# Performance work log

Hardware: AMD Instinct MI355X
Metric: run time of the kernel (lower is better)

The kernel has to match this reference:

```python
import jax, jax.numpy as jnp
import numpy as np

C, S, H = 64, 2048, 512
ITERATIONS = 3

def squash(x, eps=1e-07):
    # per-vector squash along last dim: (|x|^2/(1+|x|^2)) * x/|x|
    sq = jnp.sum(x * x, axis=-1, keepdims=True)
    safe_norm = jnp.sqrt(sq + eps)
    scale = sq / (1.0 + sq)
    return scale * (x / safe_norm)

def setup_inputs() -> dict:
    key = jax.random.key(0)
    k1, k2 = jax.random.split(key)
    x = jax.random.normal(k1, (C * S, H), dtype=jnp.float32)
    # xavier-normal init for Linear(H, H)
    std = np.sqrt(2.0 / (H + H)).astype(np.float32)
    W_weight = jax.random.normal(k2, (H, H), dtype=jnp.float32) * std
    W_bias = jnp.zeros((H,), dtype=jnp.float32)
    return {"x": x, "W_weight": W_weight, "W_bias": W_bias}

def reference(x, W_weight, W_bias):
    xr = x.reshape(C, S, H)
    # e_ij = squash(Linear(x))  -> [C, S, H]
    e_ij = squash(jnp.einsum('csh,oh->cso', xr, W_weight) + W_bias)
    b_ij = jnp.zeros((C, S), dtype=x.dtype)
    c_i = jnp.zeros((C, H), dtype=x.dtype)
    for _ in range(ITERATIONS):
        d_i = jax.nn.softmax(b_ij, axis=1)[..., None]          # [C, S, 1]
        c_i = squash(jnp.sum(d_i * e_ij, axis=1))              # [C, H]
        b_ij = b_ij + jnp.einsum('csh,ch->cs', e_ij, c_i)      # [C, S]
    return c_i
```

## Files before the change

kernel.cpp:

```cpp
#include <hip/hip_runtime.h>
#include <hip/hip_fp16.h>

#define HDIM 512

typedef __fp16 fp16x2 __attribute__((ext_vector_type(2)));
typedef _Float16 h8 __attribute__((ext_vector_type(8)));
typedef __attribute__((ext_vector_type(4))) float floatx4;

__global__ __launch_bounds__(256) void prep_w_kernel(
    const float* __restrict__ W, _Float16* __restrict__ wf) {
  int i = (blockIdx.x * 256 + threadIdx.x) * 4;
  float4 f = *(const float4*)(W + i);
  wf[i + 0] = (_Float16)f.x;
  wf[i + 1] = (_Float16)f.y;
  wf[i + 2] = (_Float16)f.z;
  wf[i + 3] = (_Float16)f.w;
}

__global__ __launch_bounds__(256) void gemm_kernel(
    const float* __restrict__ x, const _Float16* __restrict__ wf,
    const float* __restrict__ bias, __half* __restrict__ y,
    float* __restrict__ sq) {
  __shared__ _Float16 xs[128 * 64];
  __shared__ _Float16 wsm[2][128 * 64];

  const int tid = threadIdx.x;
  const int lane = tid & 63;
  const int widx = tid >> 6;
  const int wave_m = widx >> 1, wave_n = widx & 1;
  const int lrow = lane & 15, quad = lane >> 4, l7 = lane & 7;

  const int bid = blockIdx.x;
  const int m_blk = ((bid >> 5) << 3) + (bid & 7);
  const int n_blk = (bid >> 3) & 3;
  const int row0 = m_blk * 128;
  const int col0 = n_blk * 128;

  floatx4 acc[4][4];
#pragma unroll
  for (int i = 0; i < 4; ++i)
#pragma unroll
    for (int j = 0; j < 4; ++j) acc[i][j] = (floatx4){0.f, 0.f, 0.f, 0.f};

  const int xm = tid >> 3;
  const int xkg = tid & 7;
  const int wn_sub = lane >> 3;
  const int wphys = lane & 7;

  float4 xr[4][2];
  const float* xbase = x + (size_t)row0 * HDIM + xkg * 8;
#pragma unroll
  for (int p = 0; p < 4; ++p) {
    const float* gp = xbase + (size_t)(p * 32 + xm) * HDIM;
    xr[p][0] = *(const float4*)gp;
    xr[p][1] = *(const float4*)(gp + 4);
  }
#pragma unroll
  for (int q = 0; q < 4; ++q) {
    int i = widx * 4 + q;
    int n_loc = 8 * i + wn_sub;
    int kg_l = wphys ^ (n_loc & 7);
    size_t goff = (size_t)(col0 + n_loc) * HDIM + kg_l * 8;
    __builtin_amdgcn_global_load_lds(
        (const __attribute__((address_space(1))) void*)(wf + goff),
        (__attribute__((address_space(3))) void*)&wsm[0][i * 512], 16, 0, 0);
  }

  for (int kt = 0; kt < 8; ++kt) {
    __syncthreads();
#pragma unroll
    for (int p = 0; p < 4; ++p) {
      int m = p * 32 + xm;
      union { h8 v8; fp16x2 v2[4]; } u;
      u.v2[0] = __builtin_amdgcn_cvt_pkrtz(xr[p][0].x, xr[p][0].y);
      u.v2[1] = __builtin_amdgcn_cvt_pkrtz(xr[p][0].z, xr[p][0].w);
      u.v2[2] = __builtin_amdgcn_cvt_pkrtz(xr[p][1].x, xr[p][1].y);
      u.v2[3] = __builtin_amdgcn_cvt_pkrtz(xr[p][1].z, xr[p][1].w);
      int phys = xkg ^ (m & 7);
      *(h8*)&xs[m * 64 + phys * 8] = u.v8;
    }
    __syncthreads();
    if (kt < 7) {
      const int k1 = (kt + 1) * 64;
      _Float16* wdst = &wsm[(kt + 1) & 1][0];
#pragma unroll
      for (int q = 0; q < 4; ++q) {
        int i = widx * 4 + q;
        int n_loc = 8 * i + wn_sub;
        int kg_l = wphys ^ (n_loc & 7);
        size_t goff = (size_t)(col0 + n_loc) * HDIM + k1 + kg_l * 8;
        __builtin_amdgcn_global_load_lds(
            (const __attribute__((address_space(1))) void*)(wf + goff),
            (__attribute__((address_space(3))) void*)&wdst[i * 512], 16, 0, 0);
      }
#pragma unroll
      for (int p = 0; p < 4; ++p) {
        const float* gp = xbase + (size_t)(p * 32 + xm) * HDIM + k1;
        xr[p][0] = *(const float4*)gp;
        xr[p][1] = *(const float4*)(gp + 4);
      }
    }
    const _Float16* wcur = &wsm[kt & 1][0];
#pragma unroll
    for (int ks = 0; ks < 2; ++ks) {
      int physA = (ks * 4 + quad) ^ l7;
      h8 a[4], bh[4];
#pragma unroll
      for (int mt = 0; mt < 4; ++mt) {
        int r = wave_m * 64 + mt * 16 + lrow;
        a[mt] = *(const h8*)&xs[r * 64 + physA * 8];
      }
#pragma unroll
      for (int nt = 0; nt < 4; ++nt) {
        int c = wave_n * 64 + nt * 16 + lrow;
        bh[nt] = *(const h8*)&wcur[c * 64 + physA * 8];
      }
#pragma unroll
      for (int mt = 0; mt < 4; ++mt)
#pragma unroll
        for (int nt = 0; nt < 4; ++nt)
          acc[mt][nt] = __builtin_amdgcn_mfma_f32_16x16x32_f16(
              a[mt], bh[nt], acc[mt][nt], 0, 0, 0);
    }
  }

  int colg[4];
  float bias_v[4];
#pragma unroll
  for (int nt = 0; nt < 4; ++nt) {
    colg[nt] = col0 + wave_n * 64 + nt * 16 + lrow;
    bias_v[nt] = bias[colg[nt]];
  }
#pragma unroll
  for (int mt = 0; mt < 4; ++mt) {
#pragma unroll
    for (int r = 0; r < 4; ++r) {
      int rowg = row0 + wave_m * 64 + mt * 16 + quad * 4 + r;
      float s = 0.f;
#pragma unroll
      for (int nt = 0; nt < 4; ++nt) {
        float yv = acc[mt][nt][r] + bias_v[nt];
        s += yv * yv;
        y[(size_t)rowg * HDIM + colg[nt]] = __float2half(yv);
      }
      s += __shfl_xor(s, 1, 64);
      s += __shfl_xor(s, 2, 64);
      s += __shfl_xor(s, 4, 64);
      s += __shfl_xor(s, 8, 64);
      if (lrow == 0) atomicAdd(&sq[rowg], s);
    }
  }
}

__global__ __launch_bounds__(256) void kbv_kernel(
    const __half* __restrict__ y, const float* __restrict__ sqbuf,
    float* __restrict__ b, const float* __restrict__ c_buf,
    float* __restrict__ u_part, float* __restrict__ den_part) {
  const int w = threadIdx.x >> 6;
  const int lane = threadIdx.x & 63;
  const int wave_g = blockIdx.x * 4 + w;
  const int cap = wave_g >> 6;
  const int chunk = wave_g & 63;
  const int r0 = cap * 2048 + chunk * 32;

  float c8[8];
  {
    const float4* cp = (const float4*)(c_buf + cap * HDIM + lane * 8);
    float4 ca = cp[0], cb = cp[1];
    c8[0] = ca.x; c8[1] = ca.y; c8[2] = ca.z; c8[3] = ca.w;
    c8[4] = cb.x; c8[5] = cb.y; c8[6] = cb.z; c8[7] = cb.w;
  }
  float u8[8] = {0, 0, 0, 0, 0, 0, 0, 0};
  float den = 0.f;

  union U { int4 v; __half hh[8]; };
  U cur[8], nxt[8];
  const __half* yb = y + (size_t)r0 * HDIM + lane * 8;
#pragma unroll
  for (int j = 0; j < 8; ++j) cur[j].v = *(const int4*)(yb + (size_t)j * HDIM);

#pragma unroll
  for (int g = 0; g < 4; ++g) {
    const int rg = r0 + g * 8;
    if (g < 3) {
#pragma unroll
      for (int j = 0; j < 8; ++j)
        nxt[j].v = *(const int4*)(yb + (size_t)(g * 8 + 8 + j) * HDIM);
    }
    float sc[8], bv[8];
#pragma unroll
    for (int j = 0; j < 8; ++j) {
      float s = sqbuf[rg + j];
      sc[j] = s / ((1.f + s) * sqrtf(s + 1e-7f));
      bv[j] = b[rg + j];
    }
    float dot[8];
#pragma unroll
    for (int j = 0; j < 8; ++j) {
      float d = 0.f;
#pragma unroll
      for (int k = 0; k < 8; ++k) d += __half2float(cur[j].hh[k]) * c8[k];
      dot[j] = d;
    }
#pragma unroll
    for (int s = 1; s < 64; s <<= 1) {
#pragma unroll
      for (int j = 0; j < 8; ++j) dot[j] += __shfl_xor(dot[j], s, 64);
    }
#pragma unroll
    for (int j = 0; j < 8; ++j) {
      float bn = bv[j] + sc[j] * dot[j];
      if (lane == 0) b[rg + j] = bn;
      float wj = __expf(bn);
      den += wj;
      float wsc = wj * sc[j];
#pragma unroll
      for (int k = 0; k < 8; ++k) u8[k] += wsc * __half2float(cur[j].hh[k]);
    }
#pragma unroll
    for (int j = 0; j < 8; ++j) cur[j] = nxt[j];
  }

  __shared__ float lred[4][512];
  __shared__ float ldn[4];
#pragma unroll
  for (int k = 0; k < 8; ++k) lred[w][lane * 8 + k] = u8[k];
  if (lane == 0) ldn[w] = den;
  __syncthreads();
  const int t = threadIdx.x;
  const int blkc = blockIdx.x & 15;
#pragma unroll
  for (int hh = 0; hh < 2; ++hh) {
    int h = hh * 256 + t;
    float v = lred[0][h] + lred[1][h] + lred[2][h] + lred[3][h];
    u_part[((size_t)cap * 16 + blkc) * HDIM + h] = v;
  }
  if (t == 0)
    den_part[cap * 16 + blkc] = ldn[0] + ldn[1] + ldn[2] + ldn[3];
}

__global__ __launch_bounds__(512) void kcsq_kernel(
    const float* __restrict__ u_part, const float* __restrict__ den_part,
    float* __restrict__ out) {
  const int cap = blockIdx.x;
  const int t = threadIdx.x;
  __shared__ float red[512];
  __shared__ float sden;

  if (t < 16) red[t] = den_part[cap * 16 + t];
  __syncthreads();
  if (t == 0) {
    float s = 0.f;
#pragma unroll
    for (int i = 0; i < 16; ++i) s += red[i];
    sden = s;
  }
  __syncthreads();
  const float den = sden;

  float v = 0.f;
  const float* up = u_part + (size_t)cap * 16 * HDIM + t;
#pragma unroll
  for (int ch = 0; ch < 16; ++ch) v += up[ch * HDIM];
  v /= den;

  red[t] = v * v;
  __syncthreads();
  for (int s = 256; s > 0; s >>= 1) {
    if (t < s) red[t] += red[t + s];
    __syncthreads();
  }
  const float sqv = red[0];
  const float scv = sqv / ((1.f + sqv) * sqrtf(sqv + 1e-7f));
  out[cap * HDIM + t] = v * scv;
}

extern "C" void kernel_launch(void* const* d_in, const int* in_sizes, int n_in,
                              void* d_out, int out_size, void* d_ws,
                              size_t ws_size, hipStream_t stream) {
  const float* x = (const float*)d_in[0];
  const float* W = (const float*)d_in[1];
  const float* bias = (const float*)d_in[2];
  float* out = (float*)d_out;
  char* ws = (char*)d_ws;

  __half* y = (__half*)ws;
  float* sq = (float*)(ws + (size_t)134217728);
  float* b = sq + 131072;
  float* c_buf = b + 131072;
  _Float16* wf = (_Float16*)(c_buf + 32768);
  float* u_part = (float*)(wf + 262144);
  float* den_part = u_part + (size_t)64 * 16 * 512;

  (void)hipMemsetAsync(sq, 0,
                       (size_t)(131072 + 131072 + 32768) * sizeof(float),
                       stream);

  prep_w_kernel<<<256, 256, 0, stream>>>(W, wf);
  gemm_kernel<<<4096, 256, 0, stream>>>(x, wf, bias, y, sq);

  for (int it = 0; it < 3; ++it) {
    kbv_kernel<<<1024, 256, 0, stream>>>(y, sq, b, c_buf, u_part, den_part);
    kcsq_kernel<<<64, 512, 0, stream>>>(u_part, den_part,
                                        (it == 2) ? out : c_buf);
  }
}
```

Baseline: 565.8 us.

## Deepen GEMM prefetch pipeline with staggered K start and explicit waitcnt control

The GEMM now double-buffers the x register tiles two k-steps ahead, rotates each block's K starting offset by block index to spread memory traffic, and replaces __syncthreads with a raw lgkmcnt barrier plus hand-placed vmcnt waits so outstanding global loads can overlap MFMA work. The routing kernel's row batch shrinks from 8 to 4 rows per step, which lowers register pressure at the cost of more loop iterations. The hand-written vmcnt counts depend on the exact instruction count the compiler emits and could be wrong if that changes.

```diff
diff --git a/kernel.cpp b/kernel.cpp
--- a/kernel.cpp
+++ b/kernel.cpp
@@ -6,6 +6,13 @@
 typedef __fp16 fp16x2 __attribute__((ext_vector_type(2)));
 typedef _Float16 h8 __attribute__((ext_vector_type(8)));
 typedef __attribute__((ext_vector_type(4))) float floatx4;
+
+__device__ __forceinline__ void lds_barrier() {
+  asm volatile("s_waitcnt lgkmcnt(0)\n\ts_barrier" ::: "memory");
+}
+__device__ __forceinline__ void issue_fence() {
+  asm volatile("" ::: "memory");
+}
 
 __global__ __launch_bounds__(256) void prep_w_kernel(
     const float* __restrict__ W, _Float16* __restrict__ wf) {
@@ -17,6 +24,21 @@
   wf[i + 3] = (_Float16)f.w;
 }
 
+__device__ __forceinline__ void issue_w_dma(const _Float16* wf, _Float16* dst,
+                                            int col0, int kt, int widx,
+                                            int wn_sub, int wphys) {
+#pragma unroll
+  for (int q = 0; q < 4; ++q) {
+    int i = widx * 4 + q;
+    int n_loc = 8 * i + wn_sub;
+    int kg_l = wphys ^ (n_loc & 7);
+    size_t goff = (size_t)(col0 + n_loc) * HDIM + kt * 64 + kg_l * 8;
+    __builtin_amdgcn_global_load_lds(
+        (const __attribute__((address_space(1))) void*)(wf + goff),
+        (__attribute__((address_space(3))) void*)(dst + i * 512), 16, 0, 0);
+  }
+}
+
 __global__ __launch_bounds__(256) void gemm_kernel(
     const float* __restrict__ x, const _Float16* __restrict__ wf,
     const float* __restrict__ bias, __half* __restrict__ y,
@@ -35,6 +57,7 @@
   const int n_blk = (bid >> 3) & 3;
   const int row0 = m_blk * 128;
   const int col0 = n_blk * 128;
+  const int kt0 = bid & 7;
 
   floatx4 acc[4][4];
 #pragma unroll
@@ -47,60 +70,58 @@
   const int wn_sub = lane >> 3;
   const int wphys = lane & 7;
 
-  float4 xr[4][2];
   const float* xbase = x + (size_t)row0 * HDIM + xkg * 8;
+  float4 xr[2][4][2];
+
+  issue_w_dma(wf, &wsm[0][0], col0, kt0, widx, wn_sub, wphys);
+  issue_fence();
 #pragma unroll
   for (int p = 0; p < 4; ++p) {
-    const float* gp = xbase + (size_t)(p * 32 + xm) * HDIM;
-    xr[p][0] = *(const float4*)gp;
-    xr[p][1] = *(const float4*)(gp + 4);
-  }
-#pragma unroll
-  for (int q = 0; q < 4; ++q) {
-    int i = widx * 4 + q;
-    int n_loc = 8 * i + wn_sub;
-    int kg_l = wphys ^ (n_loc & 7);
-    size_t goff = (size_t)(col0 + n_loc) * HDIM + kg_l * 8;
-    __builtin_amdgcn_global_load_lds(
-        (const __attribute__((address_space(1))) void*)(wf + goff),
-        (__attribute__((address_space(3))) void*)&wsm[0][i * 512], 16, 0, 0);
-  }
-
-  for (int kt = 0; kt < 8; ++kt) {
-    __syncthreads();
+    const float* gp = xbase + (size_t)(p * 32 + xm) * HDIM + kt0 * 64;
+    xr[0][p][0] = *(const float4*)gp;
+    xr[0][p][1] = *(const float4*)(gp + 4);
+  }
+  issue_fence();
+#pragma unroll
+  for (int p = 0; p < 4; ++p) {
+    const float* gp =
+        xbase + (size_t)(p * 32 + xm) * HDIM + ((kt0 + 1) & 7) * 64;
+    xr[1][p][0] = *(const float4*)gp;
+    xr[1][p][1] = *(const float4*)(gp + 4);
+  }
+
+#pragma unroll
+  for (int i = 0; i < 8; ++i) {
+    lds_barrier();
 #pragma unroll
     for (int p = 0; p < 4; ++p) {
       int m = p * 32 + xm;
       union { h8 v8; fp16x2 v2[4]; } u;
-      u.v2[0] = __builtin_amdgcn_cvt_pkrtz(xr[p][0].x, xr[p][0].y);
-      u.v2[1] = __builtin_amdgcn_cvt_pkrtz(xr[p][0].z, xr[p][0].w);
-      u.v2[2] = __builtin_amdgcn_cvt_pkrtz(xr[p][1].x, xr[p][1].y);
-      u.v2[3] = __builtin_amdgcn_cvt_pkrtz(xr[p][1].z, xr[p][1].w);
+      u.v2[0] = __builtin_amdgcn_cvt_pkrtz(xr[i & 1][p][0].x, xr[i & 1][p][0].y);
+      u.v2[1] = __builtin_amdgcn_cvt_pkrtz(xr[i & 1][p][0].z, xr[i & 1][p][0].w);
+      u.v2[2] = __builtin_amdgcn_cvt_pkrtz(xr[i & 1][p][1].x, xr[i & 1][p][1].y);
+      u.v2[3] = __builtin_amdgcn_cvt_pkrtz(xr[i & 1][p][1].z, xr[i & 1][p][1].w);
       int phys = xkg ^ (m & 7);
       *(h8*)&xs[m * 64 + phys * 8] = u.v8;
     }
-    __syncthreads();
-    if (kt < 7) {
-      const int k1 = (kt + 1) * 64;
-      _Float16* wdst = &wsm[(kt + 1) & 1][0];
-#pragma unroll
-      for (int q = 0; q < 4; ++q) {
-        int i = widx * 4 + q;
-        int n_loc = 8 * i + wn_sub;
-        int kg_l = wphys ^ (n_loc & 7);
-        size_t goff = (size_t)(col0 + n_loc) * HDIM + k1 + kg_l * 8;
-        __builtin_amdgcn_global_load_lds(
-            (const __attribute__((address_space(1))) void*)(wf + goff),
-            (__attribute__((address_space(3))) void*)&wdst[i * 512], 16, 0, 0);
+    lds_barrier();
+    if (i < 7)
+      issue_w_dma(wf, &wsm[(i + 1) & 1][0], col0, (kt0 + i + 1) & 7, widx,
+                  wn_sub, wphys);
+    issue_fence();
+    if (i < 6) {
+      const int ktn = (kt0 + i + 2) & 7;
+#pragma unroll
+      for (int p = 0; p < 4; ++p) {
+        const float* gp = xbase + (size_t)(p * 32 + xm) * HDIM + ktn * 64;
+        xr[i & 1][p][0] = *(const float4*)gp;
+        xr[i & 1][p][1] = *(const float4*)(gp + 4);
       }
-#pragma unroll
-      for (int p = 0; p < 4; ++p) {
-        const float* gp = xbase + (size_t)(p * 32 + xm) * HDIM + k1;
-        xr[p][0] = *(const float4*)gp;
-        xr[p][1] = *(const float4*)(gp + 4);
-      }
-    }
-    const _Float16* wcur = &wsm[kt & 1][0];
+    }
+    if (i >= 1 && i <= 5) asm volatile("s_waitcnt vmcnt(20)" ::: "memory");
+    if (i == 6) asm volatile("s_waitcnt vmcnt(12)" ::: "memory");
+    if (i == 7) asm volatile("s_waitcnt vmcnt(0)" ::: "memory");
+    const _Float16* wcur = &wsm[i & 1][0];
 #pragma unroll
     for (int ks = 0; ks < 2; ++ks) {
       int physA = (ks * 4 + quad) ^ l7;
@@ -174,29 +195,28 @@
   float den = 0.f;
 
   union U { int4 v; __half hh[8]; };
-  U cur[8], nxt[8];
+  U cur[4], nxt[4];
   const __half* yb = y + (size_t)r0 * HDIM + lane * 8;
 #pragma unroll
-  for (int j = 0; j < 8; ++j) cur[j].v = *(const int4*)(yb + (size_t)j * HDIM);
-
-#pragma unroll
-  for (int g = 0; g < 4; ++g) {
-    const int rg = r0 + g * 8;
-    if (g < 3) {
-#pragma unroll
-      for (int j = 0; j < 8; ++j)
-        nxt[j].v = *(const int4*)(yb + (size_t)(g * 8 + 8 + j) * HDIM);
-    }
-    float sc[8], bv[8];
-#pragma unroll
-    for (int j = 0; j < 8; ++j) {
+  for (int j = 0; j < 4; ++j) cur[j].v = *(const int4*)(yb + (size_t)j * HDIM);
+
+  for (int g = 0; g < 8; ++g) {
+    const int rg = r0 + g * 4;
+    if (g < 7) {
+#pragma unroll
+      for (int j = 0; j < 4; ++j)
+        nxt[j].v = *(const int4*)(yb + (size_t)(g * 4 + 4 + j) * HDIM);
+    }
+    float sc[4], bv[4];
+#pragma unroll
+    for (int j = 0; j < 4; ++j) {
       float s = sqbuf[rg + j];
       sc[j] = s / ((1.f + s) * sqrtf(s + 1e-7f));
       bv[j] = b[rg + j];
     }
-    float dot[8];
-#pragma unroll
-    for (int j = 0; j < 8; ++j) {
+    float dot[4];
+#pragma unroll
+    for (int j = 0; j < 4; ++j) {
       float d = 0.f;
 #pragma unroll
       for (int k = 0; k < 8; ++k) d += __half2float(cur[j].hh[k]) * c8[k];
@@ -205,10 +225,10 @@
 #pragma unroll
     for (int s = 1; s < 64; s <<= 1) {
 #pragma unroll
-      for (int j = 0; j < 8; ++j) dot[j] += __shfl_xor(dot[j], s, 64);
-    }
-#pragma unroll
-    for (int j = 0; j < 8; ++j) {
+      for (int j = 0; j < 4; ++j) dot[j] += __shfl_xor(dot[j], s, 64);
+    }
+#pragma unroll
+    for (int j = 0; j < 4; ++j) {
       float bn = bv[j] + sc[j] * dot[j];
       if (lane == 0) b[rg + j] = bn;
       float wj = __expf(bn);
@@ -218,7 +238,7 @@
       for (int k = 0; k < 8; ++k) u8[k] += wsc * __half2float(cur[j].hh[k]);
     }
 #pragma unroll
-    for (int j = 0; j < 8; ++j) cur[j] = nxt[j];
+    for (int j = 0; j < 4; ++j) cur[j] = nxt[j];
   }
 
   __shared__ float lred[4][512];
```

Result: faster. 535.9 us (-5.3%).
